# Optimization experiments

Measured on AMD Instinct MI355X. Metric: run time of the kernel, lower is better.

Reference implementation:

```python
import jax, jax.numpy as jnp
import numpy as np

TEMPERATURE = 8.0  # sqrt(d_k=64)


def setup_inputs() -> dict:
    key = jax.random.key(0)
    kq, kk, kv = jax.random.split(key, 3)
    B, H, L, D = 4, 16, 2048, 64
    q = jax.random.normal(kq, (B, H, L, D), dtype=jnp.float32)
    k = jax.random.normal(kk, (B, H, L, D), dtype=jnp.float32)
    v = jax.random.normal(kv, (B, H, L, D), dtype=jnp.float32)
    return {"q": q, "k": k, "v": v}


def reference(q, k, v):
    # attn = softmax((q/T) @ k^T)  over last axis; dropout is identity in eval
    scores = jnp.einsum("bhqd,bhkd->bhqk", q / TEMPERATURE, k)
    attn = jax.nn.softmax(scores, axis=-1)
    out = jnp.einsum("bhqk,bhkd->bhqd", attn, v)
    return (out, attn)
```

## Files before the change

kernel.cpp:

```cpp
#include <hip/hip_runtime.h>
#include <hip/hip_bf16.h>

typedef __attribute__((ext_vector_type(4))) float  f32x4;
typedef __attribute__((ext_vector_type(8))) short  bf16x8;
typedef __attribute__((ext_vector_type(4))) short  bf16x4;

#define MFMA16(a, b, c) __builtin_amdgcn_mfma_f32_16x16x32_bf16((a), (b), (c), 0, 0, 0)

__device__ __forceinline__ short f2bf(float f) {
  return __builtin_bit_cast(short, __float2bfloat16(f));
}
__device__ __forceinline__ float bf2f(short b) {
  return __builtin_bit_cast(float, ((unsigned)(unsigned short)b) << 16);
}

__device__ __forceinline__ void sync_lds() {
  asm volatile("s_waitcnt lgkmcnt(0)" ::: "memory");
  __builtin_amdgcn_s_barrier();
  asm volatile("" ::: "memory");
}

constexpr int L = 2048, D = 64, KT = 64, NT = L / KT;
constexpr int NHEAD = 64;
constexpr int QB = 128, NQT = L / QB;
constexpr float QSCALE = 0.18033688011112042f;
constexpr size_t BF_ELEMS = (size_t)NHEAD * L * D;
constexpr size_t WS_NEED = 3 * BF_ELEMS * sizeof(short) + (size_t)NHEAD * L * sizeof(float);

__global__ __launch_bounds__(256)
void sdpa_prepV(const float* __restrict__ V, short* __restrict__ Vtb)
{
  __shared__ short Tl[64 * 72];
  const int t = threadIdx.x;
  const int head = blockIdx.x >> 5, kt = blockIdx.x & 31;
  const long base = (long)head * L * D + (long)kt * 64 * D;

  const int kr0 = (t >> 4) * 4, d0 = (t & 15) * 4;
  const float* vp = V + base;
  f32x4 r[4];
  #pragma unroll
  for (int i = 0; i < 4; ++i) r[i] = *(const f32x4*)(vp + (kr0 + i) * D + d0);
  #pragma unroll
  for (int j = 0; j < 4; ++j) {
    bf16x4 y;
    #pragma unroll
    for (int i = 0; i < 4; ++i) y[i] = f2bf(r[i][j]);
    *(bf16x4*)(&Tl[(d0 + j) * 72 + kr0]) = y;
  }
  __syncthreads();
  const int d = t >> 2, k0 = (t & 3) * 16;
  bf16x8 a = *(const bf16x8*)(&Tl[d * 72 + k0]);
  bf16x8 b = *(const bf16x8*)(&Tl[d * 72 + k0 + 8]);
  short* vo = Vtb + (long)head * D * L + (long)d * L + kt * 64 + k0;
  *(bf16x8*)vo = a; *(bf16x8*)(vo + 8) = b;
}

__global__ __launch_bounds__(256, 4)
void sdpa_rowsum2(const float* __restrict__ Qf, const float* __restrict__ Kf,
                  short* __restrict__ Qb, short* __restrict__ Kb,
                  float* __restrict__ rinv_out)
{
  __shared__ short Klds[2][KT * D];

  const int t = threadIdx.x, lane = t & 63, w = t >> 6;
  const int qr = lane & 15, g = lane >> 4;

  const int bid = blockIdx.x;
  const int wid = ((bid & 7) << 7) | (bid >> 3);
  const int head = wid >> 4, qt = wid & 15;
  const long hoff = (long)head * L * D;
  const int qrow0 = qt * QB + w * 32;

  {
    const float* qp = Qf + hoff + (long)qt * QB * D + t * 32;
    short*       qo = Qb + hoff + (long)qt * QB * D + t * 32;
    #pragma unroll
    for (int c = 0; c < 4; ++c) {
      f32x4 a = *(const f32x4*)(qp + c * 8);
      f32x4 b = *(const f32x4*)(qp + c * 8 + 4);
      bf16x8 y;
      #pragma unroll
      for (int j = 0; j < 4; ++j) {
        y[j]     = f2bf(a[j] * QSCALE);
        y[4 + j] = f2bf(b[j] * QSCALE);
      }
      *(bf16x8*)(qo + c * 8) = y;
    }
  }

  bf16x8 qfrag[2][2];
  #pragma unroll
  for (int h = 0; h < 2; ++h)
    #pragma unroll
    for (int c = 0; c < 2; ++c) {
      const float* qp = Qf + hoff + (long)(qrow0 + 16 * h + qr) * D + g * 8 + 32 * c;
      f32x4 a = *(const f32x4*)qp;
      f32x4 b = *(const f32x4*)(qp + 4);
      #pragma unroll
      for (int j = 0; j < 4; ++j) {
        qfrag[h][c][j]     = f2bf(a[j] * QSCALE);
        qfrag[h][c][4 + j] = f2bf(b[j] * QSCALE);
      }
    }

  const float* KfH = Kf + hoff;
  short*       KbH = Kb + hoff;
  const int krow = t >> 2, kd0 = (t & 3) * 16;
  f32x4 kf[4];
  bf16x8 kb0, kb1;

  auto loadK = [&](int kt) {
    const float* kp = KfH + (long)(kt * KT + krow) * D + kd0;
    #pragma unroll
    for (int i = 0; i < 4; ++i) kf[i] = *(const f32x4*)(kp + 4 * i);
  };
  auto cvtK = [&]() {
    #pragma unroll
    for (int j = 0; j < 8; ++j) {
      kb0[j] = f2bf(kf[j >> 2][j & 3]);
      kb1[j] = f2bf(kf[2 + (j >> 2)][j & 3]);
    }
  };
  auto writeKlds = [&](int buf) {
    const int sw = (krow & 7) << 3;
    *(bf16x8*)(&Klds[buf][krow * 64 + (kd0 ^ sw)])       = kb0;
    *(bf16x8*)(&Klds[buf][krow * 64 + ((kd0 + 8) ^ sw)]) = kb1;
  };
  auto maybeWriteKb = [&](int kt) {
    if ((kt >> 1) == qt) {
      short* ko = KbH + (long)(kt * KT + krow) * D + kd0;
      *(bf16x8*)ko = kb0;
      *(bf16x8*)(ko + 8) = kb1;
    }
  };

  loadK(0); cvtK(); writeKlds(0); maybeWriteKb(0);
  sync_lds();
  float rsum0 = 0.f, rsum1 = 0.f;
  for (int kt = 0; kt < NT; ++kt) {
    const int cur = kt & 1;
    if (kt + 1 < NT) loadK(kt + 1);
    #pragma unroll
    for (int f = 0; f < 4; ++f) {
      f32x4 s0 = (f32x4){0.f,0.f,0.f,0.f};
      f32x4 s1 = (f32x4){0.f,0.f,0.f,0.f};
      int kr = f * 16 + qr;
      #pragma unroll
      for (int c = 0; c < 2; ++c) {
        int d0c = g * 8 + 32 * c;
        bf16x8 a = *(const bf16x8*)(&Klds[cur][kr * 64 + (d0c ^ ((kr & 7) << 3))]);
        s0 = MFMA16(a, qfrag[0][c], s0);
        s1 = MFMA16(a, qfrag[1][c], s1);
      }
      #pragma unroll
      for (int r = 0; r < 4; ++r) {
        rsum0 += __builtin_amdgcn_exp2f(s0[r]);
        rsum1 += __builtin_amdgcn_exp2f(s1[r]);
      }
    }
    if (kt + 1 < NT) { cvtK(); writeKlds(cur ^ 1); maybeWriteKb(kt + 1); }
    sync_lds();
  }
  rsum0 += __shfl_xor(rsum0, 16); rsum0 += __shfl_xor(rsum0, 32);
  rsum1 += __shfl_xor(rsum1, 16); rsum1 += __shfl_xor(rsum1, 32);
  if (lane < 16) {
    float* ro = rinv_out + (long)head * L + qrow0;
    ro[qr]      = 1.f / rsum0;
    ro[16 + qr] = 1.f / rsum1;
  }
}

__global__ __launch_bounds__(256, 4)
void sdpa_main(const short* __restrict__ Qb, const short* __restrict__ Kb,
               const short* __restrict__ Vtb, const float* __restrict__ rinv_ws,
               float* __restrict__ out, float* __restrict__ attn)
{
  __shared__ short Klds[2][KT * D];
  __shared__ short Vlds[2][D * KT];
  __shared__ short Plds[4][16 * KT];

  const int t = threadIdx.x, lane = t & 63, w = t >> 6;
  const int qr = lane & 15, g = lane >> 4;

  const int bid = blockIdx.x;
  const int wid = ((bid & 7) << 7) | (bid >> 3);
  const int head = wid >> 4, qt = wid & 15;
  const long hoff = (long)head * L * D;
  const int qrow0 = qt * QB + w * 32;

  const float rinv0 = rinv_ws[(long)head * L + qrow0 + qr];
  const float rinv1 = rinv_ws[(long)head * L + qrow0 + 16 + qr];

  bf16x8 qfrag[2][2];
  #pragma unroll
  for (int h = 0; h < 2; ++h) {
    const short* qbp = Qb + hoff + (long)(qrow0 + 16 * h + qr) * D + g * 8;
    qfrag[h][0] = *(const bf16x8*)qbp;
    qfrag[h][1] = *(const bf16x8*)(qbp + 32);
  }

  const short* Kbase = Kb + hoff;
  const short* Vbase = Vtb + (long)head * D * L;

  bf16x8 kreg[2], vreg[2];
  const int krow = t >> 2, kd0 = (t & 3) * 16;

  auto loadK = [&](int kt) {
    const short* kp = Kbase + (long)(kt * KT + krow) * D + kd0;
    kreg[0] = *(const bf16x8*)kp;
    kreg[1] = *(const bf16x8*)(kp + 8);
  };
  auto writeK = [&](int buf) {
    const int sw = (krow & 7) << 3;
    *(bf16x8*)(&Klds[buf][krow * 64 + (kd0 ^ sw)])       = kreg[0];
    *(bf16x8*)(&Klds[buf][krow * 64 + ((kd0 + 8) ^ sw)]) = kreg[1];
  };
  auto loadV = [&](int kt) {
    const short* vp = Vbase + (long)krow * L + kt * KT + kd0;
    vreg[0] = *(const bf16x8*)vp;
    vreg[1] = *(const bf16x8*)(vp + 8);
  };
  auto writeV = [&](int buf) {
    const int sw = (krow & 7) << 3;
    *(bf16x8*)(&Vlds[buf][krow * 64 + (kd0 ^ sw)])       = vreg[0];
    *(bf16x8*)(&Vlds[buf][krow * 64 + ((kd0 + 8) ^ sw)]) = vreg[1];
  };

  auto computeS2 = [&](int buf, f32x4 s0[4], f32x4 s1[4]) {
    #pragma unroll
    for (int f = 0; f < 4; ++f) {
      s0[f] = (f32x4){0.f, 0.f, 0.f, 0.f};
      s1[f] = (f32x4){0.f, 0.f, 0.f, 0.f};
      int kr = f * 16 + qr;
      #pragma unroll
      for (int c = 0; c < 2; ++c) {
        int d0c = g * 8 + 32 * c;
        bf16x8 a = *(const bf16x8*)(&Klds[buf][kr * 64 + (d0c ^ ((kr & 7) << 3))]);
        s0[f] = MFMA16(a, qfrag[0][c], s0[f]);
        s1[f] = MFMA16(a, qfrag[1][c], s1[f]);
      }
    }
  };

  f32x4 o0[4] = {{0.f,0.f,0.f,0.f},{0.f,0.f,0.f,0.f},{0.f,0.f,0.f,0.f},{0.f,0.f,0.f,0.f}};
  f32x4 o1[4] = {{0.f,0.f,0.f,0.f},{0.f,0.f,0.f,0.f},{0.f,0.f,0.f,0.f},{0.f,0.f,0.f,0.f}};
  float* ap0 = attn + (long)head * L * L + (long)(qrow0 + qr) * L;
  float* ap1 = ap0 + 16 * L;

  auto doHalf = [&](f32x4 s[4], float rinv, float* ap, f32x4 o[4], int cur, int kt) {
    #pragma unroll
    for (int f = 0; f < 4; ++f) {
      f32x4 pf;
      #pragma unroll
      for (int r = 0; r < 4; ++r)
        pf[r] = __builtin_amdgcn_exp2f(s[f][r]) * rinv;
      *(f32x4*)(ap + kt * KT + f * 16 + g * 4) = pf;
      bf16x4 p;
      #pragma unroll
      for (int r = 0; r < 4; ++r) p[r] = f2bf(pf[r]);
      int k0 = f * 16 + g * 4;
      *(bf16x4*)(&Plds[w][qr * 64 + (k0 ^ ((qr & 7) << 3))]) = p;
    }
    __builtin_amdgcn_wave_barrier();
    #pragma unroll
    for (int kc = 0; kc < 2; ++kc) {
      int k0 = kc * 32 + g * 8;
      bf16x8 pa = *(const bf16x8*)(&Plds[w][qr * 64 + (k0 ^ ((qr & 7) << 3))]);
      #pragma unroll
      for (int fr = 0; fr < 4; ++fr) {
        int d = fr * 16 + qr;
        bf16x8 vb = *(const bf16x8*)(&Vlds[cur][d * 64 + (k0 ^ ((d & 7) << 3))]);
        o[fr] = MFMA16(pa, vb, o[fr]);
      }
    }
    __builtin_amdgcn_wave_barrier();
  };

  loadK(0); loadV(0);
  writeK(0); writeV(0);
  sync_lds();

  for (int kt = 0; kt < NT; ++kt) {
    const int cur = kt & 1;
    if (kt + 1 < NT) { loadK(kt + 1); loadV(kt + 1); }

    f32x4 s0[4], s1[4];
    computeS2(cur, s0, s1);

    doHalf(s0, rinv0, ap0, o0, cur, kt);
    doHalf(s1, rinv1, ap1, o1, cur, kt);

    if (kt + 1 < NT) { writeK(cur ^ 1); writeV(cur ^ 1); }
    sync_lds();
  }

  float* op = out + hoff + (long)qrow0 * D;
  #pragma unroll
  for (int fr = 0; fr < 4; ++fr)
    #pragma unroll
    for (int r = 0; r < 4; ++r) {
      op[(long)(g * 4 + r) * D + fr * 16 + qr]      = o0[fr][r];
      op[(long)(16 + g * 4 + r) * D + fr * 16 + qr] = o1[fr][r];
    }
}

__global__ __launch_bounds__(256, 4)
void sdpa_fused(const float* __restrict__ Q, const float* __restrict__ K,
                const float* __restrict__ V, float* __restrict__ out,
                float* __restrict__ attn)
{
  __shared__ short Klds[2][KT * D];
  __shared__ short Vlds[2][D * KT];
  __shared__ short Plds[4][16 * KT];

  const int t = threadIdx.x, lane = t & 63, w = t >> 6;
  const int qr = lane & 15, g = lane >> 4;
  const int head = blockIdx.x >> 5, qt = blockIdx.x & 31;
  const long hoff = (long)head * L * D;
  const int qrow0 = qt * 64 + w * 16;

  bf16x8 qfrag[2];
  {
    const float* qp = Q + hoff + (long)(qrow0 + qr) * D + g * 8;
    #pragma unroll
    for (int c = 0; c < 2; ++c)
      #pragma unroll
      for (int j = 0; j < 8; ++j)
        qfrag[c][j] = f2bf(qp[32 * c + j] * QSCALE);
  }

  const float* Kbase = K + hoff;
  const float* Vbase = V + hoff;
  f32x4 kreg[4], vreg[4];

  auto loadK = [&](int kt) {
    const float* kp = Kbase + (long)kt * KT * D;
    #pragma unroll
    for (int c = 0; c < 4; ++c)
      kreg[c] = *(const f32x4*)(kp + (t + 256 * c) * 4);
  };
  auto writeK = [&](int buf) {
    #pragma unroll
    for (int c = 0; c < 4; ++c) {
      int f = t + 256 * c;
      int kr = f >> 4, col = (f & 15) * 4;
      bf16x4 y;
      #pragma unroll
      for (int i = 0; i < 4; ++i) y[i] = f2bf(kreg[c][i]);
      *(bf16x4*)(&Klds[buf][kr * 64 + (col ^ ((kr & 7) << 3))]) = y;
    }
  };
  auto loadV = [&](int kt) {
    const float* vp = Vbase + (long)kt * KT * D;
    int kr0 = (t >> 4) * 4, d0 = (t & 15) * 4;
    #pragma unroll
    for (int i = 0; i < 4; ++i)
      vreg[i] = *(const f32x4*)(vp + (kr0 + i) * D + d0);
  };
  auto writeV = [&](int buf) {
    int kr0 = (t >> 4) * 4, d0 = (t & 15) * 4;
    #pragma unroll
    for (int j = 0; j < 4; ++j) {
      bf16x4 y;
      #pragma unroll
      for (int i = 0; i < 4; ++i) y[i] = f2bf(vreg[i][j]);
      int d = d0 + j;
      *(bf16x4*)(&Vlds[buf][d * 64 + (kr0 ^ ((d & 7) << 3))]) = y;
    }
  };
  auto computeS = [&](int buf, f32x4 s[4]) {
    #pragma unroll
    for (int f = 0; f < 4; ++f) {
      s[f] = (f32x4){0.f, 0.f, 0.f, 0.f};
      int kr = f * 16 + qr;
      #pragma unroll
      for (int c = 0; c < 2; ++c) {
        int d0c = g * 8 + 32 * c;
        bf16x8 a = *(const bf16x8*)(&Klds[buf][kr * 64 + (d0c ^ ((kr & 7) << 3))]);
        s[f] = MFMA16(a, qfrag[c], s[f]);
      }
    }
  };

  loadK(0); writeK(0);
  sync_lds();
  float rsum = 0.f;
  for (int kt = 0; kt < NT; ++kt) {
    const int cur = kt & 1;
    if (kt + 1 < NT) loadK(kt + 1);
    f32x4 s[4];
    computeS(cur, s);
    #pragma unroll
    for (int f = 0; f < 4; ++f)
      #pragma unroll
      for (int r = 0; r < 4; ++r)
        rsum += __builtin_amdgcn_exp2f(s[f][r]);
    if (kt + 1 < NT) writeK(cur ^ 1);
    sync_lds();
  }
  rsum += __shfl_xor(rsum, 16);
  rsum += __shfl_xor(rsum, 32);
  const float rinv = 1.f / rsum;

  f32x4 o[4] = {{0.f,0.f,0.f,0.f},{0.f,0.f,0.f,0.f},{0.f,0.f,0.f,0.f},{0.f,0.f,0.f,0.f}};
  float* ap_base = attn + (long)head * L * L + (long)qrow0 * L;

  loadK(0); loadV(0);
  writeK(0); writeV(0);
  sync_lds();

  for (int kt = 0; kt < NT; ++kt) {
    const int cur = kt & 1;
    if (kt + 1 < NT) { loadK(kt + 1); loadV(kt + 1); }

    f32x4 s[4];
    computeS(cur, s);

    #pragma unroll
    for (int f = 0; f < 4; ++f) {
      bf16x4 p;
      #pragma unroll
      for (int r = 0; r < 4; ++r)
        p[r] = f2bf(__builtin_amdgcn_exp2f(s[f][r]) * rinv);
      int k0 = f * 16 + g * 4;
      *(bf16x4*)(&Plds[w][qr * 64 + (k0 ^ ((qr & 7) << 3))]) = p;
    }
    __builtin_amdgcn_wave_barrier();

    float* ap = ap_base + (long)kt * KT;
    #pragma unroll
    for (int i = 0; i < 4; ++i) {
      int r = 4 * i + g, col = 4 * qr;
      bf16x4 pb = *(const bf16x4*)(&Plds[w][r * 64 + (col ^ ((r & 7) << 3))]);
      f32x4 pf;
      #pragma unroll
      for (int j = 0; j < 4; ++j) pf[j] = bf2f(pb[j]);
      *(f32x4*)(ap + (long)r * L + col) = pf;
    }

    #pragma unroll
    for (int kc = 0; kc < 2; ++kc) {
      int k0 = kc * 32 + g * 8;
      bf16x8 pa = *(const bf16x8*)(&Plds[w][qr * 64 + (k0 ^ ((qr & 7) << 3))]);
      #pragma unroll
      for (int fr = 0; fr < 4; ++fr) {
        int d = fr * 16 + qr;
        bf16x8 vb = *(const bf16x8*)(&Vlds[cur][d * 64 + (k0 ^ ((d & 7) << 3))]);
        o[fr] = MFMA16(pa, vb, o[fr]);
      }
    }

    if (kt + 1 < NT) { writeK(cur ^ 1); writeV(cur ^ 1); }
    sync_lds();
  }

  float* op = out + hoff + (long)qrow0 * D;
  #pragma unroll
  for (int fr = 0; fr < 4; ++fr)
    #pragma unroll
    for (int r = 0; r < 4; ++r) {
      int qq = g * 4 + r;
      op[(long)qq * D + fr * 16 + qr] = o[fr][r];
    }
}

extern "C" void kernel_launch(void* const* d_in, const int* in_sizes, int n_in,
                              void* d_out, int out_size, void* d_ws, size_t ws_size,
                              hipStream_t stream) {
  const float* q = (const float*)d_in[0];
  const float* k = (const float*)d_in[1];
  const float* v = (const float*)d_in[2];
  float* out  = (float*)d_out;
  float* attn = (float*)d_out + (size_t)NHEAD * L * D;

  dim3 block(256);

  if (ws_size >= WS_NEED) {
    short* Qb   = (short*)d_ws;
    short* Kb   = Qb + BF_ELEMS;
    short* Vtb  = Kb + BF_ELEMS;
    float* rinv = (float*)(Vtb + BF_ELEMS);
    hipLaunchKernelGGL(sdpa_prepV,   dim3(NHEAD * NT),  block, 0, stream, v, Vtb);
    hipLaunchKernelGGL(sdpa_rowsum2, dim3(NHEAD * NQT), block, 0, stream, q, k, Qb, Kb, rinv);
    hipLaunchKernelGGL(sdpa_main,    dim3(NHEAD * NQT), block, 0, stream, Qb, Kb, Vtb, rinv, out, attn);
  } else {
    hipLaunchKernelGGL(sdpa_fused, dim3(NHEAD * NT), block, 0, stream, q, k, v, out, attn);
  }
}
```

Before: 359.7 us.

## Restructure main attention kernel: persistent grid, 128-key tiles, coalesced attn stores

The main kernel becomes persistent, with 768 blocks looping over the 1024 work items. The key tile grows from 64 to 128 with single-buffered LDS instead of double-buffered, and occupancy is lowered to 3 blocks per CU. Probabilities are now written to the attn output by reading them back from LDS as bf16, so each half-wave stores contiguous row segments and the writes coalesce better. Those attn values are rounded to bf16 precision before being stored as fp32, which loses accuracy. The single buffer also adds an extra barrier per tile.

Result: faster. 312.0 us (-13.3%).

```diff
diff --git a/kernel.cpp b/kernel.cpp
--- a/kernel.cpp
+++ b/kernel.cpp
@@ -21,8 +21,10 @@
 }
 
 constexpr int L = 2048, D = 64, KT = 64, NT = L / KT;
+constexpr int KT2 = 128, NT2 = L / KT2;
 constexpr int NHEAD = 64;
 constexpr int QB = 128, NQT = L / QB;
+constexpr int GRID_MAIN = 768;
 constexpr float QSCALE = 0.18033688011112042f;
 constexpr size_t BF_ELEMS = (size_t)NHEAD * L * D;
 constexpr size_t WS_NEED = 3 * BF_ELEMS * sizeof(short) + (size_t)NHEAD * L * sizeof(float);
@@ -170,138 +172,147 @@
   }
 }
 
-__global__ __launch_bounds__(256, 4)
+__global__ __launch_bounds__(256, 3)
 void sdpa_main(const short* __restrict__ Qb, const short* __restrict__ Kb,
                const short* __restrict__ Vtb, const float* __restrict__ rinv_ws,
                float* __restrict__ out, float* __restrict__ attn)
 {
-  __shared__ short Klds[2][KT * D];
-  __shared__ short Vlds[2][D * KT];
-  __shared__ short Plds[4][16 * KT];
+  __shared__ short Klds[KT2 * D];
+  __shared__ short Vlds[D * KT2];
+  __shared__ short Plds[4][16 * KT2];
 
   const int t = threadIdx.x, lane = t & 63, w = t >> 6;
   const int qr = lane & 15, g = lane >> 4;
-
-  const int bid = blockIdx.x;
-  const int wid = ((bid & 7) << 7) | (bid >> 3);
-  const int head = wid >> 4, qt = wid & 15;
-  const long hoff = (long)head * L * D;
-  const int qrow0 = qt * QB + w * 32;
-
-  const float rinv0 = rinv_ws[(long)head * L + qrow0 + qr];
-  const float rinv1 = rinv_ws[(long)head * L + qrow0 + 16 + qr];
-
-  bf16x8 qfrag[2][2];
-  #pragma unroll
-  for (int h = 0; h < 2; ++h) {
-    const short* qbp = Qb + hoff + (long)(qrow0 + 16 * h + qr) * D + g * 8;
-    qfrag[h][0] = *(const bf16x8*)qbp;
-    qfrag[h][1] = *(const bf16x8*)(qbp + 32);
-  }
-
-  const short* Kbase = Kb + hoff;
-  const short* Vbase = Vtb + (long)head * D * L;
-
-  bf16x8 kreg[2], vreg[2];
-  const int krow = t >> 2, kd0 = (t & 3) * 16;
-
-  auto loadK = [&](int kt) {
-    const short* kp = Kbase + (long)(kt * KT + krow) * D + kd0;
-    kreg[0] = *(const bf16x8*)kp;
-    kreg[1] = *(const bf16x8*)(kp + 8);
-  };
-  auto writeK = [&](int buf) {
-    const int sw = (krow & 7) << 3;
-    *(bf16x8*)(&Klds[buf][krow * 64 + (kd0 ^ sw)])       = kreg[0];
-    *(bf16x8*)(&Klds[buf][krow * 64 + ((kd0 + 8) ^ sw)]) = kreg[1];
-  };
-  auto loadV = [&](int kt) {
-    const short* vp = Vbase + (long)krow * L + kt * KT + kd0;
-    vreg[0] = *(const bf16x8*)vp;
-    vreg[1] = *(const bf16x8*)(vp + 8);
-  };
-  auto writeV = [&](int buf) {
-    const int sw = (krow & 7) << 3;
-    *(bf16x8*)(&Vlds[buf][krow * 64 + (kd0 ^ sw)])       = vreg[0];
-    *(bf16x8*)(&Vlds[buf][krow * 64 + ((kd0 + 8) ^ sw)]) = vreg[1];
-  };
-
-  auto computeS2 = [&](int buf, f32x4 s0[4], f32x4 s1[4]) {
-    #pragma unroll
-    for (int f = 0; f < 4; ++f) {
-      s0[f] = (f32x4){0.f, 0.f, 0.f, 0.f};
-      s1[f] = (f32x4){0.f, 0.f, 0.f, 0.f};
-      int kr = f * 16 + qr;
-      #pragma unroll
-      for (int c = 0; c < 2; ++c) {
-        int d0c = g * 8 + 32 * c;
-        bf16x8 a = *(const bf16x8*)(&Klds[buf][kr * 64 + (d0c ^ ((kr & 7) << 3))]);
-        s0[f] = MFMA16(a, qfrag[0][c], s0[f]);
-        s1[f] = MFMA16(a, qfrag[1][c], s1[f]);
-      }
-    }
-  };
-
-  f32x4 o0[4] = {{0.f,0.f,0.f,0.f},{0.f,0.f,0.f,0.f},{0.f,0.f,0.f,0.f},{0.f,0.f,0.f,0.f}};
-  f32x4 o1[4] = {{0.f,0.f,0.f,0.f},{0.f,0.f,0.f,0.f},{0.f,0.f,0.f,0.f},{0.f,0.f,0.f,0.f}};
-  float* ap0 = attn + (long)head * L * L + (long)(qrow0 + qr) * L;
-  float* ap1 = ap0 + 16 * L;
-
-  auto doHalf = [&](f32x4 s[4], float rinv, float* ap, f32x4 o[4], int cur, int kt) {
-    #pragma unroll
-    for (int f = 0; f < 4; ++f) {
-      f32x4 pf;
-      #pragma unroll
-      for (int r = 0; r < 4; ++r)
-        pf[r] = __builtin_amdgcn_exp2f(s[f][r]) * rinv;
-      *(f32x4*)(ap + kt * KT + f * 16 + g * 4) = pf;
-      bf16x4 p;
-      #pragma unroll
-      for (int r = 0; r < 4; ++r) p[r] = f2bf(pf[r]);
-      int k0 = f * 16 + g * 4;
-      *(bf16x4*)(&Plds[w][qr * 64 + (k0 ^ ((qr & 7) << 3))]) = p;
-    }
-    __builtin_amdgcn_wave_barrier();
-    #pragma unroll
-    for (int kc = 0; kc < 2; ++kc) {
-      int k0 = kc * 32 + g * 8;
-      bf16x8 pa = *(const bf16x8*)(&Plds[w][qr * 64 + (k0 ^ ((qr & 7) << 3))]);
-      #pragma unroll
-      for (int fr = 0; fr < 4; ++fr) {
-        int d = fr * 16 + qr;
-        bf16x8 vb = *(const bf16x8*)(&Vlds[cur][d * 64 + (k0 ^ ((d & 7) << 3))]);
-        o[fr] = MFMA16(pa, vb, o[fr]);
-      }
-    }
-    __builtin_amdgcn_wave_barrier();
-  };
-
-  loadK(0); loadV(0);
-  writeK(0); writeV(0);
-  sync_lds();
-
-  for (int kt = 0; kt < NT; ++kt) {
-    const int cur = kt & 1;
-    if (kt + 1 < NT) { loadK(kt + 1); loadV(kt + 1); }
-
-    f32x4 s0[4], s1[4];
-    computeS2(cur, s0, s1);
-
-    doHalf(s0, rinv0, ap0, o0, cur, kt);
-    doHalf(s1, rinv1, ap1, o1, cur, kt);
-
-    if (kt + 1 < NT) { writeK(cur ^ 1); writeV(cur ^ 1); }
+  const int rlo = lane >> 5;
+
+  const int krow = t >> 1, kd0 = (t & 1) * 32;
+  const int vd   = t >> 2, vk0 = (t & 3) * 32;
+
+  for (int item = blockIdx.x; item < NHEAD * NQT; item += GRID_MAIN) {
+    const int wid = ((item & 7) << 7) | (item >> 3);
+    const int head = wid >> 4, qt = wid & 15;
+    const long hoff = (long)head * L * D;
+    const int qrow0 = qt * QB + w * 32;
+
+    const float rinv0 = rinv_ws[(long)head * L + qrow0 + qr];
+    const float rinv1 = rinv_ws[(long)head * L + qrow0 + 16 + qr];
+
+    bf16x8 qfrag[2][2];
+    #pragma unroll
+    for (int h = 0; h < 2; ++h) {
+      const short* qbp = Qb + hoff + (long)(qrow0 + 16 * h + qr) * D + g * 8;
+      qfrag[h][0] = *(const bf16x8*)qbp;
+      qfrag[h][1] = *(const bf16x8*)(qbp + 32);
+    }
+
+    const short* Kbase = Kb + hoff;
+    const short* Vbase = Vtb + (long)head * D * L;
+
+    bf16x8 kreg[4], vreg[4];
+
+    auto loadK = [&](int kt) {
+      const short* kp = Kbase + (long)(kt * KT2 + krow) * D + kd0;
+      #pragma unroll
+      for (int i = 0; i < 4; ++i) kreg[i] = *(const bf16x8*)(kp + 8 * i);
+    };
+    auto writeK = [&]() {
+      const int sw = (krow & 7) << 3;
+      #pragma unroll
+      for (int i = 0; i < 4; ++i)
+        *(bf16x8*)(&Klds[krow * 64 + ((kd0 + 8 * i) ^ sw)]) = kreg[i];
+    };
+    auto loadV = [&](int kt) {
+      const short* vp = Vbase + (long)vd * L + kt * KT2 + vk0;
+      #pragma unroll
+      for (int i = 0; i < 4; ++i) vreg[i] = *(const bf16x8*)(vp + 8 * i);
+    };
+    auto writeV = [&]() {
+      const int sw = (vd & 7) << 3;
+      #pragma unroll
+      for (int i = 0; i < 4; ++i)
+        *(bf16x8*)(&Vlds[vd * 128 + ((vk0 + 8 * i) ^ sw)]) = vreg[i];
+    };
+
+    f32x4 o0[4] = {{0.f,0.f,0.f,0.f},{0.f,0.f,0.f,0.f},{0.f,0.f,0.f,0.f},{0.f,0.f,0.f,0.f}};
+    f32x4 o1[4] = {{0.f,0.f,0.f,0.f},{0.f,0.f,0.f,0.f},{0.f,0.f,0.f,0.f},{0.f,0.f,0.f,0.f}};
+    float* apb = attn + (long)head * L * L + (long)qrow0 * L;
+
+    loadK(0); loadV(0);
     sync_lds();
-  }
-
-  float* op = out + hoff + (long)qrow0 * D;
-  #pragma unroll
-  for (int fr = 0; fr < 4; ++fr)
-    #pragma unroll
-    for (int r = 0; r < 4; ++r) {
-      op[(long)(g * 4 + r) * D + fr * 16 + qr]      = o0[fr][r];
-      op[(long)(16 + g * 4 + r) * D + fr * 16 + qr] = o1[fr][r];
-    }
+    writeK(); writeV();
+    sync_lds();
+
+    for (int kt = 0; kt < NT2; ++kt) {
+      if (kt + 1 < NT2) { loadK(kt + 1); loadV(kt + 1); }
+
+      #pragma unroll
+      for (int h = 0; h < 2; ++h) {
+        f32x4 s[8];
+        #pragma unroll
+        for (int f = 0; f < 8; ++f) {
+          s[f] = (f32x4){0.f, 0.f, 0.f, 0.f};
+          int kr = f * 16 + qr;
+          #pragma unroll
+          for (int c = 0; c < 2; ++c) {
+            int d0c = g * 8 + 32 * c;
+            bf16x8 a = *(const bf16x8*)(&Klds[kr * 64 + (d0c ^ ((kr & 7) << 3))]);
+            s[f] = MFMA16(a, qfrag[h][c], s[f]);
+          }
+        }
+        const float rinv = h ? rinv1 : rinv0;
+        #pragma unroll
+        for (int f = 0; f < 8; ++f) {
+          bf16x4 p;
+          #pragma unroll
+          for (int r = 0; r < 4; ++r)
+            p[r] = f2bf(__builtin_amdgcn_exp2f(s[f][r]) * rinv);
+          int k0 = f * 16 + g * 4;
+          *(bf16x4*)(&Plds[w][qr * 128 + (k0 ^ ((qr & 7) << 3))]) = p;
+        }
+        __builtin_amdgcn_wave_barrier();
+
+        {
+          float* ap = apb + (long)(16 * h) * L + (long)kt * KT2;
+          const int col4 = (lane & 31) * 4;
+          #pragma unroll
+          for (int i = 0; i < 8; ++i) {
+            int r = 2 * i + rlo;
+            bf16x4 pb = *(const bf16x4*)(&Plds[w][r * 128 + (col4 ^ ((r & 7) << 3))]);
+            f32x4 pf;
+            #pragma unroll
+            for (int j = 0; j < 4; ++j) pf[j] = bf2f(pb[j]);
+            *(f32x4*)(ap + (long)r * L + col4) = pf;
+          }
+        }
+
+        #pragma unroll
+        for (int kc = 0; kc < 4; ++kc) {
+          int k0 = kc * 32 + g * 8;
+          bf16x8 pa = *(const bf16x8*)(&Plds[w][qr * 128 + (k0 ^ ((qr & 7) << 3))]);
+          #pragma unroll
+          for (int fr = 0; fr < 4; ++fr) {
+            int d = fr * 16 + qr;
+            bf16x8 vb = *(const bf16x8*)(&Vlds[d * 128 + (k0 ^ ((d & 7) << 3))]);
+            if (h == 0) o0[fr] = MFMA16(pa, vb, o0[fr]);
+            else        o1[fr] = MFMA16(pa, vb, o1[fr]);
+          }
+        }
+        __builtin_amdgcn_wave_barrier();
+      }
+
+      sync_lds();
+      if (kt + 1 < NT2) { writeK(); writeV(); sync_lds(); }
+    }
+
+    float* op = out + hoff + (long)qrow0 * D;
+    #pragma unroll
+    for (int fr = 0; fr < 4; ++fr)
+      #pragma unroll
+      for (int r = 0; r < 4; ++r) {
+        op[(long)(g * 4 + r) * D + fr * 16 + qr]      = o0[fr][r];
+        op[(long)(16 + g * 4 + r) * D + fr * 16 + qr] = o1[fr][r];
+      }
+  }
 }
 
 __global__ __launch_bounds__(256, 4)
@@ -482,7 +493,7 @@
     float* rinv = (float*)(Vtb + BF_ELEMS);
     hipLaunchKernelGGL(sdpa_prepV,   dim3(NHEAD * NT),  block, 0, stream, v, Vtb);
     hipLaunchKernelGGL(sdpa_rowsum2, dim3(NHEAD * NQT), block, 0, stream, q, k, Qb, Kb, rinv);
-    hipLaunchKernelGGL(sdpa_main,    dim3(NHEAD * NQT), block, 0, stream, Qb, Kb, Vtb, rinv, out, attn);
+    hipLaunchKernelGGL(sdpa_main,    dim3(GRID_MAIN),   block, 0, stream, Qb, Kb, Vtb, rinv, out, attn);
   } else {
     hipLaunchKernelGGL(sdpa_fused, dim3(NHEAD * NT), block, 0, stream, q, k, v, out, attn);
   }
```
